# Kernel optimization log

Hardware: AMD Instinct MI355X
Metric: run time of the kernel (lower is better)

## Reference

```python
import jax, jax.numpy as jnp
import numpy as np

N = 100000
E = 1600000
E_PAIR = 100000
D_IN = 128
D_H = 128


def _sage_mean(x, src, dst, W_neigh, W_self, b):
    # DGL SAGEConv('mean'): out = fc_self(h_dst) + fc_neigh(mean_{u in N(v)} h_u) + bias
    n = x.shape[0]
    msg_sum = jax.ops.segment_sum(x[src], dst, num_segments=n)          # [N, d]
    deg = jax.ops.segment_sum(jnp.ones(src.shape, x.dtype), dst, num_segments=n)
    h_neigh = msg_sum / jnp.maximum(deg, 1.0)[:, None]
    return x @ W_self.T + h_neigh @ W_neigh.T + b


def setup_inputs() -> dict:
    key = jax.random.key(0)
    ks = jax.random.split(key, 16)
    def lin(k, fan_out, fan_in):
        s = 1.0 / np.sqrt(fan_in)
        return jax.random.uniform(k, (fan_out, fan_in), jnp.float32, -s, s)
    inp = {
        'x': jax.random.normal(ks[0], (N, D_IN), jnp.float32),
        'edge_src': jax.random.randint(ks[1], (E,), 0, N),
        'edge_dst': jax.random.randint(ks[2], (E,), 0, N),
        'pos_src': jax.random.randint(ks[3], (E_PAIR,), 0, N),
        'pos_dst': jax.random.randint(ks[4], (E_PAIR,), 0, N),
        'neg_src': jax.random.randint(ks[5], (E_PAIR,), 0, N),
        'neg_dst': jax.random.randint(ks[6], (E_PAIR,), 0, N),
        # SAGEConv layer 1 (in_feats -> n_hidden)
        'W1_neigh': lin(ks[7], D_H, D_IN),
        'W1_self': lin(ks[8], D_H, D_IN),
        'b1': jnp.zeros((D_H,), jnp.float32),
        # SAGEConv layer 2 (n_hidden -> n_hidden)
        'W2_neigh': lin(ks[9], D_H, D_H),
        'W2_self': lin(ks[10], D_H, D_H),
        'b2': jnp.zeros((D_H,), jnp.float32),
        # predictor MLP: Linear(2h->h) ReLU Linear(h->h) ReLU Linear(h->1)
        'P1_w': lin(ks[11], D_H, 2 * D_H),
        'P1_b': jnp.zeros((D_H,), jnp.float32),
        'P2_w': lin(ks[12], D_H, D_H),
        'P2_b': jnp.zeros((D_H,), jnp.float32),
        'P3_w': lin(ks[13], 1, D_H),
        'P3_b': jnp.zeros((1,), jnp.float32),
    }
    return inp


def _predict(h_src, h_dst, P1_w, P1_b, P2_w, P2_b, P3_w, P3_b):
    h = jnp.concatenate([h_src, h_dst], axis=1)
    h = jax.nn.relu(h @ P1_w.T + P1_b)
    h = jax.nn.relu(h @ P2_w.T + P2_b)
    return h @ P3_w.T + P3_b


def reference(x, edge_src, edge_dst, pos_src, pos_dst, neg_src, neg_dst,
              W1_neigh, W1_self, b1, W2_neigh, W2_self, b2,
              P1_w, P1_b, P2_w, P2_b, P3_w, P3_b):
    h = _sage_mean(x, edge_src, edge_dst, W1_neigh, W1_self, b1)
    h = jax.nn.relu(h)
    h = _sage_mean(h, edge_src, edge_dst, W2_neigh, W2_self, b2)
    h_pos = _predict(h[pos_src], h[pos_dst], P1_w, P1_b, P2_w, P2_b, P3_w, P3_b)
    h_neg = _predict(h[neg_src], h[neg_dst], P1_w, P1_b, P2_w, P2_b, P3_w, P3_b)
    return (h_pos, h_neg)
```

## Files before the change

### kernel.cpp

```cpp
#include <hip/hip_runtime.h>
#include <hip/hip_bf16.h>
#include <hip/hip_fp16.h>


#define D 128
#define NR 512
#define LDA 40
#define LDAGG 136
#define LDH2 136

typedef _Float16 f16x8 __attribute__((ext_vector_type(8)));
typedef float f32x4 __attribute__((ext_vector_type(4)));

__device__ __forceinline__ void cvt8(const float* src, _Float16* dst, int off8) {
    const float4* s4 = (const float4*)src;
    float4 a = s4[2 * off8], b = s4[2 * off8 + 1];
    f16x8 h;
    h[0] = (_Float16)a.x; h[1] = (_Float16)a.y; h[2] = (_Float16)a.z; h[3] = (_Float16)a.w;
    h[4] = (_Float16)b.x; h[5] = (_Float16)b.y; h[6] = (_Float16)b.z; h[7] = (_Float16)b.w;
    *(f16x8*)(dst + 8 * off8) = h;
}

__global__ __launch_bounds__(256) void k_setup(
    const float* __restrict__ x, _Float16* __restrict__ xf, int n8, int nb_x,
    const float* __restrict__ W1s, const float* __restrict__ W1n,
    const float* __restrict__ W2s, const float* __restrict__ W2n,
    const float* __restrict__ P1w, const float* __restrict__ P2w,
    _Float16* __restrict__ Ws1f, _Float16* __restrict__ Wn1f,
    _Float16* __restrict__ Ws2f, _Float16* __restrict__ Wn2f,
    _Float16* __restrict__ P1cf, _Float16* __restrict__ P2wf,
    const int* __restrict__ dst, int* __restrict__ region_cnt, int e, int bound) {
    int b = blockIdx.x;
    if (b < nb_x) {
        int i = b * 256 + threadIdx.x;
        if (i < n8) cvt8(x, xf, i);
        return;
    }
    b -= nb_x;
    if (b < 56) {
        int g = b * 256 + threadIdx.x;
        if (g >= 14336) return;
        if (g >= 8192 && g < 12288) {
            int u = g - 8192;
            int o = u >> 4, col = (u & 15) * 8;
            const float* src = P1w + (size_t)(o & 127) * 256 + ((o >> 7) * 128) + col;
            float4 a = *(const float4*)src, bb = *(const float4*)(src + 4);
            f16x8 h;
            h[0] = (_Float16)a.x; h[1] = (_Float16)a.y; h[2] = (_Float16)a.z; h[3] = (_Float16)a.w;
            h[4] = (_Float16)bb.x; h[5] = (_Float16)bb.y; h[6] = (_Float16)bb.z; h[7] = (_Float16)bb.w;
            *(f16x8*)(P1cf + (size_t)u * 8) = h;
            return;
        }
        const float* src; _Float16* dstp; int off;
        if      (g <  2048) { src = W1s; dstp = Ws1f; off = g; }
        else if (g <  4096) { src = W1n; dstp = Wn1f; off = g - 2048; }
        else if (g <  6144) { src = W2s; dstp = Ws2f; off = g - 4096; }
        else if (g <  8192) { src = W2n; dstp = Wn2f; off = g - 6144; }
        else                { src = P2w; dstp = P2wf; off = g - 12288; }
        cvt8(src, dstp, off);
        return;
    }
    b -= 56;
    __shared__ int s[NR];
    for (int i = threadIdx.x; i < NR; i += 256) s[i] = 0;
    __syncthreads();
    for (int i = b * 256 + threadIdx.x; i < e; i += 128 * 256)
        atomicAdd(&s[dst[i] / bound], 1);
    __syncthreads();
    for (int i = threadIdx.x; i < NR; i += 256)
        if (s[i]) atomicAdd(&region_cnt[i], s[i]);
}

__global__ __launch_bounds__(NR) void k_regbase(
    const int* __restrict__ region_cnt,
    int* __restrict__ region_base, int* __restrict__ region_cursor) {
    __shared__ int s[NR];
    int t = threadIdx.x;
    int v = region_cnt[t];
    s[t] = v;
    __syncthreads();
    #pragma unroll
    for (int off = 1; off < NR; off <<= 1) {
        int add = (t >= off) ? s[t - off] : 0;
        __syncthreads();
        s[t] += add;
        __syncthreads();
    }
    int ex = s[t] - v;
    region_base[t] = ex;
    region_cursor[t] = ex;
    if (t == NR - 1) region_base[NR] = s[t];
}

__global__ __launch_bounds__(256) void k_regpart(
    const int* __restrict__ src, const int* __restrict__ dst,
    unsigned int* __restrict__ eout, int* __restrict__ region_cursor, int e, int bound) {
    __shared__ int s_cnt[NR];
    __shared__ int s_base[NR];
    int per = (e + gridDim.x - 1) / gridDim.x;
    int beg = blockIdx.x * per;
    int end = min(beg + per, e);
    for (int i = threadIdx.x; i < NR; i += 256) s_cnt[i] = 0;
    __syncthreads();
    for (int i = beg + threadIdx.x; i < end; i += 256)
        atomicAdd(&s_cnt[dst[i] / bound], 1);
    __syncthreads();
    for (int i = threadIdx.x; i < NR; i += 256)
        s_base[i] = s_cnt[i] ? atomicAdd(&region_cursor[i], s_cnt[i]) : 0;
    __syncthreads();
    for (int i = threadIdx.x; i < NR; i += 256) s_cnt[i] = 0;
    __syncthreads();
    for (int i = beg + threadIdx.x; i < end; i += 256) {
        int d = dst[i];
        int r = d / bound;
        unsigned int doff = (unsigned int)(d - r * bound);
        int p = atomicAdd(&s_cnt[r], 1);
        eout[s_base[r] + p] = (unsigned int)src[i] | (doff << 20);
    }
}

#define EMAX 4608
__global__ __launch_bounds__(256) void k_rowoff_scatter(
    const unsigned int* __restrict__ ep, const int* __restrict__ region_base,
    int* __restrict__ row_off, int* __restrict__ csr, int n, int bound) {
    int r = blockIdx.x;
    int rlo = r * bound;
    if (threadIdx.x == 0 && r == 0) row_off[n] = region_base[NR];
    if (rlo >= n) return;
    int nn = min(bound, n - rlo);
    __shared__ unsigned int s_e[EMAX];
    __shared__ int s_deg[256];
    __shared__ int s_scan[256];
    __shared__ int s_cur[256];
    int beg = region_base[r], end = region_base[r + 1];
    int cnt = end - beg;
    bool fit = (cnt <= EMAX);
    if (fit)
        for (int i = threadIdx.x; i < cnt; i += 256) s_e[i] = ep[beg + i];
    s_deg[threadIdx.x] = 0;
    __syncthreads();
    for (int i = threadIdx.x; i < cnt; i += 256)
        atomicAdd(&s_deg[(fit ? s_e[i] : ep[beg + i]) >> 20], 1);
    __syncthreads();
    int v = (threadIdx.x < nn) ? s_deg[threadIdx.x] : 0;
    s_scan[threadIdx.x] = v;
    __syncthreads();
    #pragma unroll
    for (int off = 1; off < 256; off <<= 1) {
        int add = (threadIdx.x >= off) ? s_scan[threadIdx.x - off] : 0;
        __syncthreads();
        s_scan[threadIdx.x] += add;
        __syncthreads();
    }
    int base = beg + (threadIdx.x ? s_scan[threadIdx.x - 1] : 0);
    s_cur[threadIdx.x] = base;
    if (threadIdx.x < nn) row_off[rlo + threadIdx.x] = base;
    __syncthreads();
    for (int i = threadIdx.x; i < cnt; i += 256) {
        unsigned int e2 = fit ? s_e[i] : ep[beg + i];
        int doff = e2 >> 20;
        int p = atomicAdd(&s_cur[doff], 1);
        csr[p] = e2 & 0xFFFFF;
    }
}

__global__ __launch_bounds__(256) void k_agg(
    const _Float16* __restrict__ Xf, const int* __restrict__ row_off,
    const int* __restrict__ csr, _Float16* __restrict__ Aggf, int n_nodes) {
    int g = blockIdx.x * 16 + (threadIdx.x >> 4);
    if (g >= n_nodes) return;
    int l = threadIdx.x & 15;
    int beg = row_off[g], end = row_off[g + 1];
    float acc[8] = {0.f, 0.f, 0.f, 0.f, 0.f, 0.f, 0.f, 0.f};
    int i = beg;
    for (; i + 8 <= end; i += 8) {
        int si[8];
        #pragma unroll
        for (int j = 0; j < 8; ++j) si[j] = csr[i + j];
        f16x8 vv[8];
        #pragma unroll
        for (int j = 0; j < 8; ++j)
            vv[j] = *(const f16x8*)(Xf + (size_t)si[j] * D + l * 8);
        #pragma unroll
        for (int j = 0; j < 8; ++j)
            #pragma unroll
            for (int k = 0; k < 8; ++k) acc[k] += (float)vv[j][k];
    }
    for (; i + 2 <= end; i += 2) {
        int s0 = csr[i], s1 = csr[i + 1];
        f16x8 v0 = *(const f16x8*)(Xf + (size_t)s0 * D + l * 8);
        f16x8 v1 = *(const f16x8*)(Xf + (size_t)s1 * D + l * 8);
        #pragma unroll
        for (int k = 0; k < 8; ++k) acc[k] += (float)v0[k] + (float)v1[k];
    }
    if (i < end) {
        int s0 = csr[i];
        f16x8 v0 = *(const f16x8*)(Xf + (size_t)s0 * D + l * 8);
        #pragma unroll
        for (int k = 0; k < 8; ++k) acc[k] += (float)v0[k];
    }
    float inv = 1.0f / fmaxf((float)(end - beg), 1.0f);
    f16x8 o;
    #pragma unroll
    for (int k = 0; k < 8; ++k) o[k] = (_Float16)(acc[k] * inv);
    *(f16x8*)(Aggf + (size_t)g * D + l * 8) = o;
}

__global__ __launch_bounds__(512) void k_transform(
    const _Float16* __restrict__ Xf, const _Float16* __restrict__ Aggf,
    const _Float16* __restrict__ Wsf, const _Float16* __restrict__ Wnf,
    const float* __restrict__ bias, _Float16* __restrict__ outf, int n_rows) {
    __shared__ _Float16 s_a[2][128 * LDA];
    __shared__ _Float16 s_b[2][128 * LDA];
    int tid = threadIdx.x;
    int w = tid >> 6, l = tid & 63;
    int wr = w >> 1, wc = w & 1;
    int l15 = l & 15, lk = l >> 4;
    int n0 = blockIdx.x * 128;
    int r = tid >> 2, q = tid & 3;
    int rstage = n0 + r; if (rstage >= n_rows) rstage = n_rows - 1;

    f32x4 acc[2][4];
    #pragma unroll
    for (int i = 0; i < 2; ++i)
        #pragma unroll
        for (int j = 0; j < 4; ++j) acc[i][j] = (f32x4){0.f, 0.f, 0.f, 0.f};

    int a_off = (wr * 32 + l15) * LDA + lk * 8;
    int b_off = (wc * 64 + l15) * LDA + lk * 8;
    int st_off = r * LDA + q * 8;

    {
        f16x8 av = *(const f16x8*)(Xf + (size_t)rstage * D + q * 8);
        f16x8 wv = *(const f16x8*)(Wsf + (size_t)r * D + q * 8);
        *(f16x8*)(&s_a[0][st_off]) = av;
        *(f16x8*)(&s_b[0][st_off]) = wv;
    }
    __syncthreads();

    for (int c = 0; c < 8; ++c) {
        int b = c & 1;
        f16x8 av, wv;
        if (c < 7) {
            int cn = c + 1;
            const _Float16* asrc = (cn < 4) ? Xf : Aggf;
            const _Float16* wsrc = (cn < 4) ? Wsf : Wnf;
            int kb = (cn & 3) * 32;
            av = *(const f16x8*)(asrc + (size_t)rstage * D + kb + q * 8);
            wv = *(const f16x8*)(wsrc + (size_t)r * D + kb + q * 8);
        }
        f16x8 af[2], bf[4];
        af[0] = *(const f16x8*)(&s_a[b][a_off]);
        af[1] = *(const f16x8*)(&s_a[b][a_off + 16 * LDA]);
        #pragma unroll
        for (int j = 0; j < 4; ++j) bf[j] = *(const f16x8*)(&s_b[b][b_off + j * 16 * LDA]);
        #pragma unroll
        for (int i = 0; i < 2; ++i)
            #pragma unroll
            for (int j = 0; j < 4; ++j)
                acc[i][j] = __builtin_amdgcn_mfma_f32_16x16x32_f16(af[i], bf[j], acc[i][j], 0, 0, 0);
        if (c < 7) {
            *(f16x8*)(&s_a[b ^ 1][st_off]) = av;
            *(f16x8*)(&s_b[b ^ 1][st_off]) = wv;
        }
        __syncthreads();
    }

    #pragma unroll
    for (int j = 0; j < 4; ++j) {
        int col = wc * 64 + j * 16 + l15;
        float bv = bias[col];
        #pragma unroll
        for (int i = 0; i < 2; ++i) {
            int rowb = n0 + wr * 32 + i * 16 + lk * 4;
            #pragma unroll
            for (int v = 0; v < 4; ++v) {
                int row = rowb + v;
                if (row < n_rows)
                    outf[(size_t)row * D + col] = (_Float16)fmaxf(acc[i][j][v] + bv, 0.f);
            }
        }
    }
}

__global__ __launch_bounds__(512) void k_transform_pre(
    const _Float16* __restrict__ Xf, const _Float16* __restrict__ Aggf,
    const _Float16* __restrict__ Wsf, const _Float16* __restrict__ Wnf,
    const float* __restrict__ bias, const _Float16* __restrict__ P1cf,
    _Float16* __restrict__ Pre, int n_rows) {
    __shared__ _Float16 s_a[2][128 * LDA];
    __shared__ _Float16 s_b[2][128 * LDA];
    __shared__ _Float16 s_h2[128 * LDAGG];
    int tid = threadIdx.x;
    int w = tid >> 6, l = tid & 63;
    int l15 = l & 15, lk = l >> 4;
    int n0 = blockIdx.x * 128;
    int r = tid >> 2, q = tid & 3;
    int rstage = n0 + r; if (rstage >= n_rows) rstage = n_rows - 1;

    {
        int wr = w >> 1, wc = w & 1;
        f32x4 acc[2][4];
        #pragma unroll
        for (int i = 0; i < 2; ++i)
            #pragma unroll
            for (int j = 0; j < 4; ++j) acc[i][j] = (f32x4){0.f, 0.f, 0.f, 0.f};

        int a_off = (wr * 32 + l15) * LDA + lk * 8;
        int b_off = (wc * 64 + l15) * LDA + lk * 8;
        int st_off = r * LDA + q * 8;

        f16x8 av0 = *(const f16x8*)(Xf + (size_t)rstage * D + q * 8);
        f16x8 wv0 = *(const f16x8*)(Wsf + (size_t)r * D + q * 8);
        *(f16x8*)(&s_a[0][st_off]) = av0;
        *(f16x8*)(&s_b[0][st_off]) = wv0;
        __syncthreads();

        for (int c = 0; c < 8; ++c) {
            int b = c & 1;
            f16x8 av, wv;
            if (c < 7) {
                int cn = c + 1;
                const _Float16* asrc = (cn < 4) ? Xf : Aggf;
                const _Float16* wsrc = (cn < 4) ? Wsf : Wnf;
                int kb = (cn & 3) * 32;
                av = *(const f16x8*)(asrc + (size_t)rstage * D + kb + q * 8);
                wv = *(const f16x8*)(wsrc + (size_t)r * D + kb + q * 8);
            }
            f16x8 af[2], bf[4];
            af[0] = *(const f16x8*)(&s_a[b][a_off]);
            af[1] = *(const f16x8*)(&s_a[b][a_off + 16 * LDA]);
            #pragma unroll
            for (int j = 0; j < 4; ++j) bf[j] = *(const f16x8*)(&s_b[b][b_off + j * 16 * LDA]);
            #pragma unroll
            for (int i = 0; i < 2; ++i)
                #pragma unroll
                for (int j = 0; j < 4; ++j)
                    acc[i][j] = __builtin_amdgcn_mfma_f32_16x16x32_f16(af[i], bf[j], acc[i][j], 0, 0, 0);
            if (c < 7) {
                *(f16x8*)(&s_a[b ^ 1][st_off]) = av;
                *(f16x8*)(&s_b[b ^ 1][st_off]) = wv;
            }
            __syncthreads();
        }

        #pragma unroll
        for (int j = 0; j < 4; ++j) {
            int col = wc * 64 + j * 16 + l15;
            float bv = bias[col];
            #pragma unroll
            for (int i = 0; i < 2; ++i) {
                int rowb = wr * 32 + i * 16 + lk * 4;
                #pragma unroll
                for (int v = 0; v < 4; ++v)
                    s_h2[(rowb + v) * LDAGG + col] = (_Float16)(acc[i][j][v] + bv);
            }
        }
    }

    {
        int wr = w >> 2, wc = w & 3;
        _Float16* s_flat = &s_a[0][0];
        f32x4 acc2[4][4];
        #pragma unroll
        for (int i = 0; i < 4; ++i)
            #pragma unroll
            for (int j = 0; j < 4; ++j) acc2[i][j] = (f32x4){0.f, 0.f, 0.f, 0.f};

        for (int c2 = 0; c2 < 4; ++c2) {
            __syncthreads();
            #pragma unroll
            for (int e = 0; e < 2; ++e) {
                int idx = tid + e * 512;
                int o = idx >> 2, qq = idx & 3;
                *(f16x8*)(&s_flat[o * LDA + qq * 8]) =
                    *(const f16x8*)(P1cf + (size_t)o * 128 + c2 * 32 + qq * 8);
            }
            __syncthreads();
            f16x8 af[4], bf[4];
            #pragma unroll
            for (int i = 0; i < 4; ++i)
                af[i] = *(const f16x8*)(&s_h2[(wr * 64 + i * 16 + l15) * LDAGG + c2 * 32 + lk * 8]);
            #pragma unroll
            for (int j = 0; j < 4; ++j)
                bf[j] = *(const f16x8*)(&s_flat[(wc * 64 + j * 16 + l15) * LDA + lk * 8]);
            #pragma unroll
            for (int i = 0; i < 4; ++i)
                #pragma unroll
                for (int j = 0; j < 4; ++j)
                    acc2[i][j] = __builtin_amdgcn_mfma_f32_16x16x32_f16(af[i], bf[j], acc2[i][j], 0, 0, 0);
        }

        #pragma unroll
        for (int j = 0; j < 4; ++j) {
            int col = wc * 64 + j * 16 + l15;
            #pragma unroll
            for (int i = 0; i < 4; ++i) {
                int rowb = n0 + wr * 64 + i * 16 + lk * 4;
                #pragma unroll
                for (int v = 0; v < 4; ++v) {
                    int row = rowb + v;
                    if (row < n_rows)
                        Pre[(size_t)row * 256 + col] = (_Float16)acc2[i][j][v];
                }
            }
        }
    }
}

__global__ __launch_bounds__(256) void k_mlp(
    const _Float16* __restrict__ Pre,
    const int* __restrict__ pos_src, const int* __restrict__ pos_dst,
    const int* __restrict__ neg_src, const int* __restrict__ neg_dst,
    const float* __restrict__ P1b,
    const _Float16* __restrict__ P2wf, const float* __restrict__ P2b,
    const float* __restrict__ P3w, const float* __restrict__ P3b,
    float* __restrict__ out, int EP) {
    __shared__ _Float16 s_h1[64 * LDH2];
    __shared__ _Float16 s_b[2][128 * LDA];
    __shared__ float s_red[64 * 2];
    __shared__ int s_node[128];
    int tid = threadIdx.x;
    int w = tid >> 6, l = tid & 63;
    int wr = w >> 1, wc = w & 1;
    int l15 = l & 15, lk = l >> 4;
    int p0 = blockIdx.x * 64;
    int twoEP = 2 * EP;

    if (tid < 128) {
        int p = p0 + (tid & 63);
        if (p >= twoEP) p = twoEP - 1;
        int node;
        if (tid < 64) node = (p < EP) ? pos_src[p] : neg_src[p - EP];
        else          node = (p < EP) ? pos_dst[p] : neg_dst[p - EP];
        s_node[tid] = node;
    }
    __syncthreads();

    #pragma unroll
    for (int e = 0; e < 4; ++e) {
        int idx = tid + e * 256;
        int pr = idx >> 4, u = idx & 15;
        int sn = s_node[pr], dn = s_node[64 + pr];
        f16x8 a = *(const f16x8*)(Pre + (size_t)sn * 256 + u * 8);
        f16x8 b = *(const f16x8*)(Pre + (size_t)dn * 256 + 128 + u * 8);
        float4 b0 = *(const float4*)(P1b + u * 8);
        float4 b1 = *(const float4*)(P1b + u * 8 + 4);
        float bb[8] = {b0.x, b0.y, b0.z, b0.w, b1.x, b1.y, b1.z, b1.w};
        f16x8 h;
        #pragma unroll
        for (int j = 0; j < 8; ++j)
            h[j] = (_Float16)fmaxf((float)a[j] + (float)b[j] + bb[j], 0.f);
        *(f16x8*)(&s_h1[pr * LDH2 + u * 8]) = h;
    }
    #pragma unroll
    for (int e = 0; e < 2; ++e) {
        int idx = tid + e * 256;
        int o = idx >> 2, q = idx & 3;
        *(f16x8*)(&s_b[0][o * LDA + q * 8]) = *(const f16x8*)(P2wf + (size_t)o * D + q * 8);
    }
    __syncthreads();

    f32x4 acc2[2][4];
    #pragma unroll
    for (int i = 0; i < 2; ++i)
        #pragma unroll
        for (int j = 0; j < 4; ++j) acc2[i][j] = (f32x4){0.f, 0.f, 0.f, 0.f};

    for (int c = 0; c < 4; ++c) {
        int b = c & 1;
        f16x8 nw[2];
        if (c < 3) {
            #pragma unroll
            for (int e = 0; e < 2; ++e) {
                int idx = tid + e * 256;
                int o = idx >> 2, q = idx & 3;
                nw[e] = *(const f16x8*)(P2wf + (size_t)o * D + (c + 1) * 32 + q * 8);
            }
        }
        f16x8 af[2], bf[4];
        af[0] = *(const f16x8*)(&s_h1[(wr * 32 + l15) * LDH2 + c * 32 + lk * 8]);
        af[1] = *(const f16x8*)(&s_h1[(wr * 32 + 16 + l15) * LDH2 + c * 32 + lk * 8]);
        #pragma unroll
        for (int j = 0; j < 4; ++j)
            bf[j] = *(const f16x8*)(&s_b[b][(wc * 64 + j * 16 + l15) * LDA + lk * 8]);
        #pragma unroll
        for (int i = 0; i < 2; ++i)
            #pragma unroll
            for (int j = 0; j < 4; ++j)
                acc2[i][j] = __builtin_amdgcn_mfma_f32_16x16x32_f16(af[i], bf[j], acc2[i][j], 0, 0, 0);
        if (c < 3) {
            #pragma unroll
            for (int e = 0; e < 2; ++e) {
                int idx = tid + e * 256;
                int o = idx >> 2, q = idx & 3;
                *(f16x8*)(&s_b[b ^ 1][o * LDA + q * 8]) = nw[e];
            }
        }
        __syncthreads();
    }

    float b2v[4], pw[4];
    #pragma unroll
    for (int j = 0; j < 4; ++j) {
        int col = wc * 64 + j * 16 + l15;
        b2v[j] = P2b[col];
        pw[j] = P3w[col];
    }
    #pragma unroll
    for (int i = 0; i < 2; ++i) {
        #pragma unroll
        for (int v = 0; v < 4; ++v) {
            float s = 0.f;
            #pragma unroll
            for (int j = 0; j < 4; ++j)
                s += fmaxf(acc2[i][j][v] + b2v[j], 0.f) * pw[j];
            s += __shfl_xor(s, 1);
            s += __shfl_xor(s, 2);
            s += __shfl_xor(s, 4);
            s += __shfl_xor(s, 8);
            if (l15 == 0)
                s_red[(wr * 32 + i * 16 + lk * 4 + v) * 2 + wc] = s;
        }
    }
    __syncthreads();
    if (tid < 64) {
        int p = p0 + tid;
        if (p < twoEP) out[p] = s_red[tid * 2] + s_red[tid * 2 + 1] + P3b[0];
    }
}

static inline size_t align_up(size_t x, size_t a) { return (x + a - 1) & ~(a - 1); }

extern "C" void kernel_launch(void* const* d_in, const int* in_sizes, int n_in,
                              void* d_out, int out_size, void* d_ws, size_t ws_size,
                              hipStream_t stream) {
    const float* x        = (const float*)d_in[0];
    const int*   edge_src = (const int*)d_in[1];
    const int*   edge_dst = (const int*)d_in[2];
    const int*   pos_src  = (const int*)d_in[3];
    const int*   pos_dst  = (const int*)d_in[4];
    const int*   neg_src  = (const int*)d_in[5];
    const int*   neg_dst  = (const int*)d_in[6];
    const float* W1n = (const float*)d_in[7];
    const float* W1s = (const float*)d_in[8];
    const float* b1  = (const float*)d_in[9];
    const float* W2n = (const float*)d_in[10];
    const float* W2s = (const float*)d_in[11];
    const float* b2  = (const float*)d_in[12];
    const float* P1w = (const float*)d_in[13];
    const float* P1b = (const float*)d_in[14];
    const float* P2w = (const float*)d_in[15];
    const float* P2b = (const float*)d_in[16];
    const float* P3w = (const float*)d_in[17];
    const float* P3b = (const float*)d_in[18];
    float* out = (float*)d_out;

    const int N = in_sizes[0] / D;
    const int E = in_sizes[1];
    const int EP = in_sizes[3];
    const int bound = (N + NR - 1) / NR;

    char* ws = (char*)d_ws;
    size_t off = 0;
    int* row_off = (int*)(ws + off); off = align_up(off + (size_t)(N + 1) * 4, 256);
    int* regmeta = (int*)(ws + off); off = align_up(off + (size_t)(3 * NR + 8) * 4, 256);
    int* csr     = (int*)(ws + off); off = align_up(off + (size_t)E * 4, 256);
    unsigned int* epart = (unsigned int*)(ws + off); off = align_up(off + (size_t)E * 4, 256);
    _Float16* xf   = (_Float16*)(ws + off); off = align_up(off + (size_t)N * D * 2, 256);
    _Float16* aggf = (_Float16*)(ws + off); off = align_up(off + (size_t)N * D * 2, 256);
    _Float16* h1f  = (_Float16*)(ws + off); off = align_up(off + (size_t)N * D * 2, 256);
    _Float16* Pre  = (_Float16*)(ws + off); off = align_up(off + (size_t)N * 256 * 2, 256);
    _Float16* Ws1f = (_Float16*)(ws + off); off = align_up(off + (size_t)D * D * 2, 256);
    _Float16* Wn1f = (_Float16*)(ws + off); off = align_up(off + (size_t)D * D * 2, 256);
    _Float16* Ws2f = (_Float16*)(ws + off); off = align_up(off + (size_t)D * D * 2, 256);
    _Float16* Wn2f = (_Float16*)(ws + off); off = align_up(off + (size_t)D * D * 2, 256);
    _Float16* P1cf = (_Float16*)(ws + off); off = align_up(off + (size_t)2 * D * D * 2, 256);
    _Float16* P2wf = (_Float16*)(ws + off); off = align_up(off + (size_t)D * D * 2, 256);
    (void)ws_size;

    int* region_cnt    = regmeta;
    int* region_base   = regmeta + NR;
    int* region_cursor = regmeta + 2 * NR + 4;

    const int n8 = N * D / 8;
    const int nb_x = (n8 + 255) / 256;

    hipMemsetAsync(region_cnt, 0, NR * 4, stream);
    k_setup<<<nb_x + 56 + 128, 256, 0, stream>>>(
        x, xf, n8, nb_x, W1s, W1n, W2s, W2n, P1w, P2w,
        Ws1f, Wn1f, Ws2f, Wn2f, P1cf, P2wf,
        edge_dst, region_cnt, E, bound);
    k_regbase<<<1, NR, 0, stream>>>(region_cnt, region_base, region_cursor);
    k_regpart<<<128, 256, 0, stream>>>(edge_src, edge_dst, epart, region_cursor, E, bound);
    k_rowoff_scatter<<<NR, 256, 0, stream>>>(epart, region_base, row_off, csr, N, bound);

    const int ngrid = (N + 127) / 128;
    const int pgrid = (2 * EP + 63) / 64;

    k_agg<<<(N + 15) / 16, 256, 0, stream>>>(xf, row_off, csr, aggf, N);
    k_transform<<<ngrid, 512, 0, stream>>>(xf, aggf, Ws1f, Wn1f, b1, h1f, N);
    k_agg<<<(N + 15) / 16, 256, 0, stream>>>(h1f, row_off, csr, aggf, N);
    k_transform_pre<<<ngrid, 512, 0, stream>>>(h1f, aggf, Ws2f, Wn2f, b2, P1cf, Pre, N);

    k_mlp<<<pgrid, 256, 0, stream>>>(Pre, pos_src, pos_dst, neg_src, neg_dst,
                                     P1b, P2wf, P2b, P3w, P3b, out, EP);
}
```

Baseline: 303.5 us.

## Fuse CSR-building kernels into one cooperative kernel with grid syncs

Merges the setup/conversion, region histogram, region scan, partition and per-region scatter kernels into a single cooperative launch of NR blocks separated by grid.sync(). Each block recomputes the region prefix scan redundantly in shared memory instead of launching a separate scan kernel. This removes several kernel launches and the gaps between them. In exchange, the fp16 conversion of x now runs on only 512 blocks via a grid-stride loop instead of a large grid, the kernel depends on all 512 blocks being co-resident, and the larger shared-memory footprint may lower occupancy.

```diff
diff --git a/kernel.cpp b/kernel.cpp
--- a/kernel.cpp
+++ b/kernel.cpp
@@ -1,10 +1,14 @@
 #include <hip/hip_runtime.h>
 #include <hip/hip_bf16.h>
 #include <hip/hip_fp16.h>
-
+#include <hip/hip_cooperative_groups.h>
+
+
+namespace cg = cooperative_groups;
 
 #define D 128
 #define NR 512
+#define EMAX 4608
 #define LDA 40
 #define LDAGG 136
 #define LDH2 136
@@ -21,25 +25,34 @@
     *(f16x8*)(dst + 8 * off8) = h;
 }
 
-__global__ __launch_bounds__(256) void k_setup(
-    const float* __restrict__ x, _Float16* __restrict__ xf, int n8, int nb_x,
+__global__ __launch_bounds__(256) void k_csr(
+    const float* __restrict__ x, _Float16* __restrict__ xf, int n8,
     const float* __restrict__ W1s, const float* __restrict__ W1n,
     const float* __restrict__ W2s, const float* __restrict__ W2n,
     const float* __restrict__ P1w, const float* __restrict__ P2w,
     _Float16* __restrict__ Ws1f, _Float16* __restrict__ Wn1f,
     _Float16* __restrict__ Ws2f, _Float16* __restrict__ Wn2f,
     _Float16* __restrict__ P1cf, _Float16* __restrict__ P2wf,
-    const int* __restrict__ dst, int* __restrict__ region_cnt, int e, int bound) {
-    int b = blockIdx.x;
-    if (b < nb_x) {
-        int i = b * 256 + threadIdx.x;
-        if (i < n8) cvt8(x, xf, i);
-        return;
-    }
-    b -= nb_x;
-    if (b < 56) {
-        int g = b * 256 + threadIdx.x;
-        if (g >= 14336) return;
+    const int* __restrict__ esrc, const int* __restrict__ edst,
+    unsigned int* __restrict__ epart, int* __restrict__ csr,
+    int* __restrict__ row_off, int* __restrict__ region_cnt,
+    int* __restrict__ cursor2, int n, int e, int bound) {
+    cg::grid_group grid = cg::this_grid();
+    __shared__ int s_h[NR];
+    __shared__ int s_base[NR];
+    __shared__ int s_cntA[NR];
+    __shared__ int s_resv[NR];
+    __shared__ unsigned int s_e[EMAX];
+    __shared__ int s_deg[256];
+    __shared__ int s_scan[256];
+    __shared__ int s_cur[256];
+    int tid = threadIdx.x;
+    int bid = blockIdx.x;
+    int gstride = gridDim.x * 256;
+    int gtid = bid * 256 + tid;
+
+    for (int i = gtid; i < n8; i += gstride) cvt8(x, xf, i);
+    for (int g = gtid; g < 14336; g += gstride) {
         if (g >= 8192 && g < 12288) {
             int u = g - 8192;
             int o = u >> 4, col = (u & 15) * 8;
@@ -49,118 +62,107 @@
             h[0] = (_Float16)a.x; h[1] = (_Float16)a.y; h[2] = (_Float16)a.z; h[3] = (_Float16)a.w;
             h[4] = (_Float16)bb.x; h[5] = (_Float16)bb.y; h[6] = (_Float16)bb.z; h[7] = (_Float16)bb.w;
             *(f16x8*)(P1cf + (size_t)u * 8) = h;
-            return;
-        }
-        const float* src; _Float16* dstp; int off;
-        if      (g <  2048) { src = W1s; dstp = Ws1f; off = g; }
-        else if (g <  4096) { src = W1n; dstp = Wn1f; off = g - 2048; }
-        else if (g <  6144) { src = W2s; dstp = Ws2f; off = g - 4096; }
-        else if (g <  8192) { src = W2n; dstp = Wn2f; off = g - 6144; }
-        else                { src = P2w; dstp = P2wf; off = g - 12288; }
-        cvt8(src, dstp, off);
-        return;
-    }
-    b -= 56;
-    __shared__ int s[NR];
-    for (int i = threadIdx.x; i < NR; i += 256) s[i] = 0;
+        } else {
+            const float* src; _Float16* dstp; int off;
+            if      (g <  2048) { src = W1s; dstp = Ws1f; off = g; }
+            else if (g <  4096) { src = W1n; dstp = Wn1f; off = g - 2048; }
+            else if (g <  6144) { src = W2s; dstp = Ws2f; off = g - 4096; }
+            else if (g <  8192) { src = W2n; dstp = Wn2f; off = g - 6144; }
+            else                { src = P2w; dstp = P2wf; off = g - 12288; }
+            cvt8(src, dstp, off);
+        }
+    }
+    for (int i = tid; i < NR; i += 256) s_h[i] = 0;
     __syncthreads();
-    for (int i = b * 256 + threadIdx.x; i < e; i += 128 * 256)
-        atomicAdd(&s[dst[i] / bound], 1);
+    for (int i = gtid; i < e; i += gstride)
+        atomicAdd(&s_h[edst[i] / bound], 1);
     __syncthreads();
-    for (int i = threadIdx.x; i < NR; i += 256)
-        if (s[i]) atomicAdd(&region_cnt[i], s[i]);
-}
-
-__global__ __launch_bounds__(NR) void k_regbase(
-    const int* __restrict__ region_cnt,
-    int* __restrict__ region_base, int* __restrict__ region_cursor) {
-    __shared__ int s[NR];
-    int t = threadIdx.x;
-    int v = region_cnt[t];
-    s[t] = v;
-    __syncthreads();
-    #pragma unroll
-    for (int off = 1; off < NR; off <<= 1) {
-        int add = (t >= off) ? s[t - off] : 0;
-        __syncthreads();
-        s[t] += add;
-        __syncthreads();
-    }
-    int ex = s[t] - v;
-    region_base[t] = ex;
-    region_cursor[t] = ex;
-    if (t == NR - 1) region_base[NR] = s[t];
-}
-
-__global__ __launch_bounds__(256) void k_regpart(
-    const int* __restrict__ src, const int* __restrict__ dst,
-    unsigned int* __restrict__ eout, int* __restrict__ region_cursor, int e, int bound) {
-    __shared__ int s_cnt[NR];
-    __shared__ int s_base[NR];
-    int per = (e + gridDim.x - 1) / gridDim.x;
-    int beg = blockIdx.x * per;
-    int end = min(beg + per, e);
-    for (int i = threadIdx.x; i < NR; i += 256) s_cnt[i] = 0;
-    __syncthreads();
-    for (int i = beg + threadIdx.x; i < end; i += 256)
-        atomicAdd(&s_cnt[dst[i] / bound], 1);
-    __syncthreads();
-    for (int i = threadIdx.x; i < NR; i += 256)
-        s_base[i] = s_cnt[i] ? atomicAdd(&region_cursor[i], s_cnt[i]) : 0;
-    __syncthreads();
-    for (int i = threadIdx.x; i < NR; i += 256) s_cnt[i] = 0;
-    __syncthreads();
-    for (int i = beg + threadIdx.x; i < end; i += 256) {
-        int d = dst[i];
-        int r = d / bound;
-        unsigned int doff = (unsigned int)(d - r * bound);
-        int p = atomicAdd(&s_cnt[r], 1);
-        eout[s_base[r] + p] = (unsigned int)src[i] | (doff << 20);
-    }
-}
-
-#define EMAX 4608
-__global__ __launch_bounds__(256) void k_rowoff_scatter(
-    const unsigned int* __restrict__ ep, const int* __restrict__ region_base,
-    int* __restrict__ row_off, int* __restrict__ csr, int n, int bound) {
-    int r = blockIdx.x;
-    int rlo = r * bound;
-    if (threadIdx.x == 0 && r == 0) row_off[n] = region_base[NR];
-    if (rlo >= n) return;
-    int nn = min(bound, n - rlo);
-    __shared__ unsigned int s_e[EMAX];
-    __shared__ int s_deg[256];
-    __shared__ int s_scan[256];
-    __shared__ int s_cur[256];
-    int beg = region_base[r], end = region_base[r + 1];
-    int cnt = end - beg;
-    bool fit = (cnt <= EMAX);
-    if (fit)
-        for (int i = threadIdx.x; i < cnt; i += 256) s_e[i] = ep[beg + i];
-    s_deg[threadIdx.x] = 0;
-    __syncthreads();
-    for (int i = threadIdx.x; i < cnt; i += 256)
-        atomicAdd(&s_deg[(fit ? s_e[i] : ep[beg + i]) >> 20], 1);
-    __syncthreads();
-    int v = (threadIdx.x < nn) ? s_deg[threadIdx.x] : 0;
-    s_scan[threadIdx.x] = v;
-    __syncthreads();
-    #pragma unroll
-    for (int off = 1; off < 256; off <<= 1) {
-        int add = (threadIdx.x >= off) ? s_scan[threadIdx.x - off] : 0;
-        __syncthreads();
-        s_scan[threadIdx.x] += add;
-        __syncthreads();
-    }
-    int base = beg + (threadIdx.x ? s_scan[threadIdx.x - 1] : 0);
-    s_cur[threadIdx.x] = base;
-    if (threadIdx.x < nn) row_off[rlo + threadIdx.x] = base;
-    __syncthreads();
-    for (int i = threadIdx.x; i < cnt; i += 256) {
-        unsigned int e2 = fit ? s_e[i] : ep[beg + i];
-        int doff = e2 >> 20;
-        int p = atomicAdd(&s_cur[doff], 1);
-        csr[p] = e2 & 0xFFFFF;
+    for (int i = tid; i < NR; i += 256)
+        if (s_h[i]) atomicAdd(&region_cnt[i], s_h[i]);
+
+    grid.sync();
+
+    {
+        int c0 = region_cnt[tid], c1 = region_cnt[tid + 256];
+        s_cntA[tid] = c0; s_cntA[tid + 256] = c1;
+        s_base[tid] = c0; s_base[tid + 256] = c1;
+        __syncthreads();
+        #pragma unroll
+        for (int off = 1; off < NR; off <<= 1) {
+            int t2 = tid + 256;
+            int v0 = (tid >= off) ? s_base[tid - off] : 0;
+            int v1 = (t2 >= off) ? s_base[t2 - off] : 0;
+            __syncthreads();
+            s_base[tid] += v0; s_base[t2] += v1;
+            __syncthreads();
+        }
+        int e0 = s_base[tid] - s_cntA[tid];
+        int e1 = s_base[tid + 256] - s_cntA[tid + 256];
+        __syncthreads();
+        s_base[tid] = e0; s_base[tid + 256] = e1;
+        __syncthreads();
+    }
+
+    {
+        int per = (e + gridDim.x - 1) / gridDim.x;
+        int beg = bid * per, end = min(beg + per, e);
+        for (int i = tid; i < NR; i += 256) s_h[i] = 0;
+        __syncthreads();
+        for (int i = beg + tid; i < end; i += 256)
+            atomicAdd(&s_h[edst[i] / bound], 1);
+        __syncthreads();
+        for (int i = tid; i < NR; i += 256)
+            s_resv[i] = s_base[i] + (s_h[i] ? atomicAdd(&cursor2[i], s_h[i]) : 0);
+        __syncthreads();
+        for (int i = tid; i < NR; i += 256) s_h[i] = 0;
+        __syncthreads();
+        for (int i = beg + tid; i < end; i += 256) {
+            int d = edst[i];
+            int r = d / bound;
+            unsigned int doff = (unsigned int)(d - r * bound);
+            int p = atomicAdd(&s_h[r], 1);
+            epart[s_resv[r] + p] = (unsigned int)esrc[i] | (doff << 20);
+        }
+    }
+
+    grid.sync();
+
+    {
+        int r = bid;
+        int rlo = r * bound;
+        if (tid == 0 && r == 0) row_off[n] = s_base[NR - 1] + s_cntA[NR - 1];
+        if (rlo >= n) return;
+        int nn = min(bound, n - rlo);
+        int beg = s_base[r];
+        int cnt = s_cntA[r];
+        bool fit = (cnt <= EMAX);
+        if (fit)
+            for (int i = tid; i < cnt; i += 256) s_e[i] = epart[beg + i];
+        s_deg[tid] = 0;
+        __syncthreads();
+        for (int i = tid; i < cnt; i += 256)
+            atomicAdd(&s_deg[(fit ? s_e[i] : epart[beg + i]) >> 20], 1);
+        __syncthreads();
+        int v = (tid < nn) ? s_deg[tid] : 0;
+        s_scan[tid] = v;
+        __syncthreads();
+        #pragma unroll
+        for (int off = 1; off < 256; off <<= 1) {
+            int add = (tid >= off) ? s_scan[tid - off] : 0;
+            __syncthreads();
+            s_scan[tid] += add;
+            __syncthreads();
+        }
+        int base = beg + (tid ? s_scan[tid - 1] : 0);
+        s_cur[tid] = base;
+        if (tid < nn) row_off[rlo + tid] = base;
+        __syncthreads();
+        for (int i = tid; i < cnt; i += 256) {
+            unsigned int e2 = fit ? s_e[i] : epart[beg + i];
+            int doff = e2 >> 20;
+            int p = atomicAdd(&s_cur[doff], 1);
+            csr[p] = e2 & 0xFFFFF;
+        }
     }
 }
 
@@ -556,15 +558,15 @@
     const float* P3b = (const float*)d_in[18];
     float* out = (float*)d_out;
 
-    const int N = in_sizes[0] / D;
-    const int E = in_sizes[1];
-    const int EP = in_sizes[3];
-    const int bound = (N + NR - 1) / NR;
+    int N = in_sizes[0] / D;
+    int E = in_sizes[1];
+    int EP = in_sizes[3];
+    int bound = (N + NR - 1) / NR;
 
     char* ws = (char*)d_ws;
     size_t off = 0;
     int* row_off = (int*)(ws + off); off = align_up(off + (size_t)(N + 1) * 4, 256);
-    int* regmeta = (int*)(ws + off); off = align_up(off + (size_t)(3 * NR + 8) * 4, 256);
+    int* regmeta = (int*)(ws + off); off = align_up(off + (size_t)(2 * NR) * 4, 256);
     int* csr     = (int*)(ws + off); off = align_up(off + (size_t)E * 4, 256);
     unsigned int* epart = (unsigned int*)(ws + off); off = align_up(off + (size_t)E * 4, 256);
     _Float16* xf   = (_Float16*)(ws + off); off = align_up(off + (size_t)N * D * 2, 256);
@@ -579,21 +581,27 @@
     _Float16* P2wf = (_Float16*)(ws + off); off = align_up(off + (size_t)D * D * 2, 256);
     (void)ws_size;
 
-    int* region_cnt    = regmeta;
-    int* region_base   = regmeta + NR;
-    int* region_cursor = regmeta + 2 * NR + 4;
-
-    const int n8 = N * D / 8;
-    const int nb_x = (n8 + 255) / 256;
-
-    hipMemsetAsync(region_cnt, 0, NR * 4, stream);
-    k_setup<<<nb_x + 56 + 128, 256, 0, stream>>>(
-        x, xf, n8, nb_x, W1s, W1n, W2s, W2n, P1w, P2w,
-        Ws1f, Wn1f, Ws2f, Wn2f, P1cf, P2wf,
-        edge_dst, region_cnt, E, bound);
-    k_regbase<<<1, NR, 0, stream>>>(region_cnt, region_base, region_cursor);
-    k_regpart<<<128, 256, 0, stream>>>(edge_src, edge_dst, epart, region_cursor, E, bound);
-    k_rowoff_scatter<<<NR, 256, 0, stream>>>(epart, region_base, row_off, csr, N, bound);
+    int* region_cnt = regmeta;
+    int* cursor2    = regmeta + NR;
+
+    int n8 = N * D / 8;
+
+    hipMemsetAsync(regmeta, 0, 2 * NR * 4, stream);
+    {
+        void* args[] = {
+            (void*)&x, (void*)&xf, (void*)&n8,
+            (void*)&W1s, (void*)&W1n, (void*)&W2s, (void*)&W2n,
+            (void*)&P1w, (void*)&P2w,
+            (void*)&Ws1f, (void*)&Wn1f, (void*)&Ws2f, (void*)&Wn2f,
+            (void*)&P1cf, (void*)&P2wf,
+            (void*)&edge_src, (void*)&edge_dst,
+            (void*)&epart, (void*)&csr, (void*)&row_off,
+            (void*)&region_cnt, (void*)&cursor2,
+            (void*)&N, (void*)&E, (void*)&bound
+        };
+        hipLaunchCooperativeKernel((const void*)k_csr, dim3(NR), dim3(256),
+                                   args, 0, stream);
+    }
 
     const int ngrid = (N + 127) / 128;
     const int pgrid = (2 * EP + 63) / 64;
```

Measured after the change: 411.9 us. +35.8%, slower.
